# Optimization experiments

Measured on AMD Instinct MI355X. Metric: run time of the kernel, lower is better.

Reference implementation:

```python
import jax, jax.numpy as jnp
import numpy as np

EMBED_DIM = 768
NUM_HEADS = 12


def setup_inputs() -> dict:
    key = jax.random.key(0)
    ks = jax.random.split(key, 9)
    B, N, C = 16, 1024, EMBED_DIM
    std = 1.0 / np.sqrt(C)
    x = jax.random.normal(ks[0], (B, N, C), dtype=jnp.float32)
    def w(k):
        return jax.random.normal(k, (C, C), dtype=jnp.float32) * std
    def b(k):
        return jax.random.normal(k, (C,), dtype=jnp.float32) * 0.01
    return {
        "x": x,
        "Wq": w(ks[1]), "bq": b(ks[2]),
        "Wk": w(ks[3]), "bk": b(ks[4]),
        "Wv": w(ks[5]), "bv": b(ks[6]),
        "Wo": w(ks[7]), "bo": b(ks[8]),
    }


def reference(x, Wq, bq, Wk, bk, Wv, bv, Wo, bo):
    B, N, C = x.shape
    H = NUM_HEADS
    Dh = C // H
    scale = 1.0 / np.sqrt(Dh)

    q = x @ Wq + bq  # (B, N, C)
    k = x @ Wk + bk
    v = x @ Wv + bv

    # Faithful to the original: (B, N, H, Dh) -> reshape(B*H, N, Dh)
    # WITHOUT transposing, exactly as torch_mla_core does (row-major reshape).
    q2 = q.reshape(B * H, N, Dh)
    k2 = k.reshape(B * H, N, Dh)
    v2 = v.reshape(B * H, N, Dh)

    scores = jnp.einsum('gld,gmd->glm', q2, k2) * scale  # (B*H, N, N)
    attn = jax.nn.softmax(scores, axis=-1)
    ctx2 = jnp.einsum('glm,gmd->gld', attn, v2)  # (B*H, N, Dh)

    ctx = ctx2.reshape(B, H, N, Dh).transpose(0, 2, 1, 3).reshape(B, N, C)
    out = ctx @ Wo + bo
    return out
```

## Files before the change

### kernel.cpp

```cpp
#include <hip/hip_runtime.h>
#include <hip/hip_bf16.h>
#include <cstdint>
#include <cstddef>

typedef unsigned short u16;
typedef __attribute__((ext_vector_type(8))) short s8v;
typedef __attribute__((ext_vector_type(4))) float f4v;
typedef __attribute__((ext_vector_type(8))) u16 u16x8;
typedef __attribute__((ext_vector_type(4))) uint32_t u32x4;

#define AS1 __attribute__((address_space(1)))
#define AS3 __attribute__((address_space(3)))

#define BATCH 16
#define SEQ   1024
#define EMBED 768
#define HEADS 12
#define DH    64
#define MTOT  (BATCH*SEQ)

__device__ __forceinline__ u16 f2bf(float f) {
    union { float f; uint32_t u; } v; v.f = f;
    uint32_t r = v.u + 0x7fffu + ((v.u >> 16) & 1u);
    return (u16)(r >> 16);
}

__device__ __forceinline__ void gll16(const u16* g, u16* l) {
    __builtin_amdgcn_global_load_lds((AS1 void*)g, (AS3 void*)l, 16, 0, 0);
}

#define XBLOCKS 12288
#define TBLOCKS 576
__global__ void k_pack(const float* __restrict__ x, u16* __restrict__ xb, int nx,
                       const float* __restrict__ Wq, const float* __restrict__ Wk,
                       const float* __restrict__ Wv, const float* __restrict__ Wo,
                       const float* __restrict__ bq, const float* __restrict__ bk,
                       const float* __restrict__ bv,
                       u16* __restrict__ wqkvT, u16* __restrict__ woT,
                       float* __restrict__ bqkv)
{
    __shared__ __attribute__((aligned(16))) u16 ts[64 * 80];
    const int tid = threadIdx.x;
    if (blockIdx.x < XBLOCKS) {
        int i = (blockIdx.x * 256 + tid) * 4;
        if (i + 3 < nx) {
            float4 f = *(const float4*)(x + i);
            ushort4 o;
            o.x = f2bf(f.x); o.y = f2bf(f.y); o.z = f2bf(f.z); o.w = f2bf(f.w);
            *(ushort4*)(xb + i) = o;
        }
        return;
    }
    int tb = blockIdx.x - XBLOCKS;
    if (tb < TBLOCKS) {
        const float* src; u16* dst; int n0, k0, nn0; float sc;
        if (tb < 432) {
            int nt = tb % 36, kt = tb / 36;
            n0 = nt * 64; k0 = kt * 64; dst = wqkvT;
            if (n0 < 768)       { src = Wq; nn0 = n0;        sc = 0.125f; }
            else if (n0 < 1536) { src = Wk; nn0 = n0 - 768;  sc = 1.0f;   }
            else                { src = Wv; nn0 = n0 - 1536; sc = 1.0f;   }
        } else {
            int tb2 = tb - 432;
            int nt = tb2 % 12, kt = tb2 / 12;
            n0 = nt * 64; k0 = kt * 64; nn0 = n0; sc = 1.0f;
            src = Wo; dst = woT;
        }
        const int r = tid >> 2, cb = (tid & 3) * 16;
#pragma unroll
        for (int i = 0; i < 4; ++i) {
            float4 f = *(const float4*)(src + (size_t)(k0 + r) * 768 + nn0 + cb + i * 4);
            ts[(cb + i * 4 + 0) * 80 + r] = f2bf(f.x * sc);
            ts[(cb + i * 4 + 1) * 80 + r] = f2bf(f.y * sc);
            ts[(cb + i * 4 + 2) * 80 + r] = f2bf(f.z * sc);
            ts[(cb + i * 4 + 3) * 80 + r] = f2bf(f.w * sc);
        }
        __syncthreads();
#pragma unroll
        for (int j = 0; j < 2; ++j) {
            u16x8 tv = *(const u16x8*)(ts + r * 80 + cb + j * 8);
            *(u16x8*)(dst + (size_t)(n0 + r) * 768 + k0 + cb + j * 8) = tv;
        }
        return;
    }
    int t3 = (tb - TBLOCKS) * 256 + tid;
    if (t3 < 2304) {
        bqkv[t3] = (t3 < 768) ? bq[t3] * 0.125f
                 : ((t3 < 1536) ? bk[t3 - 768] : bv[t3 - 1536]);
    }
}

template<int MODE>
__global__ __launch_bounds__(256) void k_gemm(
    const u16* __restrict__ A, const u16* __restrict__ BT,
    const float* __restrict__ bias,
    u16* __restrict__ oq, u16* __restrict__ okk, u16* __restrict__ ov,
    float* __restrict__ of)
{
    __shared__ __attribute__((aligned(16))) u16 As[128 * 64];
    __shared__ __attribute__((aligned(16))) u16 Bs[128 * 64];
    const int tid = threadIdx.x;
    const int m0 = blockIdx.x * 128;
    const int n0 = blockIdx.y * 128;
    const int wv = tid >> 6;
    const int ln = tid & 63;
    const int l15 = ln & 15, quad = ln >> 4;
    const int wm = (wv >> 1) * 64, wn = (wv & 1) * 64;

    const int srow = tid >> 3;
    const int schnk = ((tid & 7) ^ (srow & 7)) * 8;
    const u16* gA = A + (size_t)(m0 + srow) * 768 + schnk;
    const u16* gB = BT + (size_t)(n0 + srow) * 768 + schnk;
    u16* lA = As + wv * 512;
    u16* lB = Bs + wv * 512;

    const int sl0 = ((quad)     ^ (l15 & 7)) * 8;
    const int sl1 = ((4 + quad) ^ (l15 & 7)) * 8;

    f4v acc[4][4] = {};

    for (int kt = 0; kt < 12; ++kt) {
        const int ko = kt * 64;
#pragma unroll
        for (int i = 0; i < 4; ++i) {
            gll16(gA + (size_t)i * 32 * 768 + ko, lA + i * 2048);
            gll16(gB + (size_t)i * 32 * 768 + ko, lB + i * 2048);
        }
        __syncthreads();

        s8v aF[4][2];
#pragma unroll
        for (int i = 0; i < 4; ++i) {
            const u16* base = As + (wm + i * 16 + l15) * 64;
            aF[i][0] = *(const s8v*)(base + sl0);
            aF[i][1] = *(const s8v*)(base + sl1);
        }
#pragma unroll
        for (int j = 0; j < 4; ++j) {
            const u16* base = Bs + (wn + j * 16 + l15) * 64;
            s8v bF0 = *(const s8v*)(base + sl0);
            s8v bF1 = *(const s8v*)(base + sl1);
#pragma unroll
            for (int i = 0; i < 4; ++i) {
                acc[i][j] = __builtin_amdgcn_mfma_f32_16x16x32_bf16(aF[i][0], bF0, acc[i][j], 0, 0, 0);
                acc[i][j] = __builtin_amdgcn_mfma_f32_16x16x32_bf16(aF[i][1], bF1, acc[i][j], 0, 0, 0);
            }
        }
        __syncthreads();
    }

#pragma unroll
    for (int j = 0; j < 4; ++j) {
        int n = n0 + wn + j * 16 + l15;
        float bs = bias[n];
        if (MODE == 0) {
            u16* dst; int nn;
            if (n < 768)       { dst = oq;  nn = n; }
            else if (n < 1536) { dst = okk; nn = n - 768; }
            else               { dst = ov;  nn = n - 1536; }
#pragma unroll
            for (int i = 0; i < 4; ++i) {
                int mrow = m0 + wm + i * 16 + quad * 4;
#pragma unroll
                for (int rg = 0; rg < 4; ++rg)
                    dst[(size_t)(mrow + rg) * 768 + nn] = f2bf(acc[i][j][rg] + bs);
            }
        } else {
#pragma unroll
            for (int i = 0; i < 4; ++i) {
                int mrow = m0 + wm + i * 16 + quad * 4;
#pragma unroll
                for (int rg = 0; rg < 4; ++rg)
                    of[(size_t)(mrow + rg) * 768 + n] = acc[i][j][rg] + bs;
            }
        }
    }
}

__global__ void k_transpose_v(const u16* __restrict__ v, u16* __restrict__ vt) {
    __shared__ __attribute__((aligned(16))) u16 ts[64 * 80];
    int g = blockIdx.x >> 4;
    int l0 = (blockIdx.x & 15) << 6;
    const u16* vg = v + (size_t)g * 65536;
    u16* vtg = vt + (size_t)g * 65536;
    int tid = threadIdx.x;
#pragma unroll
    for (int c = tid; c < 512; c += 256) {
        int l = c >> 3, d0 = (c & 7) * 8;
        *(uint4*)(ts + l * 80 + d0) = *(const uint4*)(vg + (size_t)(l0 + l) * 64 + d0);
    }
    __syncthreads();
#pragma unroll
    for (int c = tid; c < 512; c += 256) {
        int d = c >> 3, lc = (c & 7) * 8;
        u16x8 tv;
#pragma unroll
        for (int i = 0; i < 8; ++i) tv[i] = ts[(lc + i) * 80 + d];
        *(u16x8*)(vtg + (size_t)d * 1024 + l0 + lc) = tv;
    }
}

#define KS2(r_, c_) ( ((r_) << 6) + (((((c_) >> 3) ^ ((r_) & 7)) & 7) << 3) + ((c_) & 7) )

__global__ __launch_bounds__(256) void k_attn(
    const u16* __restrict__ qb, const u16* __restrict__ kb,
    const u16* __restrict__ vt, u16* __restrict__ ctx)
{
    __shared__ __attribute__((aligned(16))) u16 Ks[128 * 64];
    __shared__ __attribute__((aligned(16))) u16 Vts[64 * 136];

    const int g = blockIdx.x >> 3;
    const int q0 = (blockIdx.x & 7) << 7;
    const int tid = threadIdx.x, wv = tid >> 6;
    const int ln = tid & 63, l15 = ln & 15, quad = ln >> 4;
    const u16* qg = qb + (size_t)g * 65536;
    const u16* kg = kb + (size_t)g * 65536;
    const u16* vtg = vt + (size_t)g * 65536;

    const int krr = tid >> 3, kcb = (tid & 7) * 8;
    const int vd = tid >> 4, vc0 = (tid & 15) * 8;
    const u16* kgp = kg + (size_t)krr * 64 + kcb;
    const u16* vgp = vtg + (size_t)vd * 1024 + vc0;

    uint4 kr0 = *(const uint4*)(kgp);
    uint4 kr1 = *(const uint4*)(kgp + 2048);
    uint4 kr2 = *(const uint4*)(kgp + 4096);
    uint4 kr3 = *(const uint4*)(kgp + 6144);
    uint4 vr0 = *(const uint4*)(vgp);
    uint4 vr1 = *(const uint4*)(vgp + 16384);
    uint4 vr2 = *(const uint4*)(vgp + 32768);
    uint4 vr3 = *(const uint4*)(vgp + 49152);

    const u16* qrow = qg + (size_t)(q0 + wv * 32 + l15) * 64 + quad * 8;
    s8v aQ00 = *(const s8v*)qrow;
    s8v aQ01 = *(const s8v*)(qrow + 32);
    s8v aQ10 = *(const s8v*)(qrow + 1024);
    s8v aQ11 = *(const s8v*)(qrow + 1024 + 32);

    f4v o0[4] = {}, o1[4] = {};
    float rsum0 = 0.f, rsum1 = 0.f;

    for (int jt = 0; jt < 8; ++jt) {
        __builtin_amdgcn_s_barrier();
        __builtin_amdgcn_sched_barrier(0);

        *(uint4*)(Ks + KS2(krr,      kcb)) = kr0;
        *(uint4*)(Ks + KS2(krr + 32, kcb)) = kr1;
        *(uint4*)(Ks + KS2(krr + 64, kcb)) = kr2;
        *(uint4*)(Ks + KS2(krr + 96, kcb)) = kr3;
        *(uint4*)(Vts + (vd     ) * 136 + vc0) = vr0;
        *(uint4*)(Vts + (vd + 16) * 136 + vc0) = vr1;
        *(uint4*)(Vts + (vd + 32) * 136 + vc0) = vr2;
        *(uint4*)(Vts + (vd + 48) * 136 + vc0) = vr3;

        if (jt < 7) {
            const size_t koff = (size_t)(jt + 1) * 8192;
            const int voff = (jt + 1) * 128;
            kr0 = *(const uint4*)(kgp + koff);
            kr1 = *(const uint4*)(kgp + koff + 2048);
            kr2 = *(const uint4*)(kgp + koff + 4096);
            kr3 = *(const uint4*)(kgp + koff + 6144);
            vr0 = *(const uint4*)(vgp + voff);
            vr1 = *(const uint4*)(vgp + voff + 16384);
            vr2 = *(const uint4*)(vgp + voff + 32768);
            vr3 = *(const uint4*)(vgp + voff + 49152);
        }

        asm volatile("s_waitcnt lgkmcnt(0)" ::: "memory");
        __builtin_amdgcn_s_barrier();
        __builtin_amdgcn_sched_barrier(0);

        f4v s0[8], s1[8];
        __builtin_amdgcn_s_setprio(1);
#pragma unroll
        for (int ns = 0; ns < 8; ++ns) {
            int rK = ns * 16 + l15;
            s8v b0 = *(const s8v*)(Ks + KS2(rK, quad * 8));
            s8v b1 = *(const s8v*)(Ks + KS2(rK, quad * 8 + 32));
            f4v t0 = {};
            t0 = __builtin_amdgcn_mfma_f32_16x16x32_bf16(b0, aQ00, t0, 0, 0, 0);
            t0 = __builtin_amdgcn_mfma_f32_16x16x32_bf16(b1, aQ01, t0, 0, 0, 0);
            s0[ns] = t0;
            f4v t1 = {};
            t1 = __builtin_amdgcn_mfma_f32_16x16x32_bf16(b0, aQ10, t1, 0, 0, 0);
            t1 = __builtin_amdgcn_mfma_f32_16x16x32_bf16(b1, aQ11, t1, 0, 0, 0);
            s1[ns] = t1;
        }
        __builtin_amdgcn_s_setprio(0);

        s8v aP0[4], aP1[4];
#pragma unroll
        for (int ns = 0; ns < 8; ++ns)
#pragma unroll
            for (int rg = 0; rg < 4; ++rg) {
                float p = __expf(s0[ns][rg]);
                s0[ns][rg] = p;
                rsum0 += p;
            }
#pragma unroll
        for (int ks = 0; ks < 4; ++ks) {
            uint32_t a0, a1, c0, c1;
            asm("v_cvt_pk_bf16_f32 %0, %1, %2" : "=v"(a0) : "v"(s0[2*ks][0]),   "v"(s0[2*ks][1]));
            asm("v_cvt_pk_bf16_f32 %0, %1, %2" : "=v"(a1) : "v"(s0[2*ks][2]),   "v"(s0[2*ks][3]));
            asm("v_cvt_pk_bf16_f32 %0, %1, %2" : "=v"(c0) : "v"(s0[2*ks+1][0]), "v"(s0[2*ks+1][1]));
            asm("v_cvt_pk_bf16_f32 %0, %1, %2" : "=v"(c1) : "v"(s0[2*ks+1][2]), "v"(s0[2*ks+1][3]));
            asm("v_permlane32_swap_b32 %0, %1" : "+v"(a0), "+v"(c0));
            asm("v_permlane16_swap_b32 %0, %1" : "+v"(a0), "+v"(c0));
            asm("v_permlane32_swap_b32 %0, %1" : "+v"(a1), "+v"(c1));
            asm("v_permlane16_swap_b32 %0, %1" : "+v"(a1), "+v"(c1));
            u32x4 pk; pk.x = a0; pk.y = a1; pk.z = c0; pk.w = c1;
            aP0[ks] = __builtin_bit_cast(s8v, pk);
        }
#pragma unroll
        for (int ns = 0; ns < 8; ++ns)
#pragma unroll
            for (int rg = 0; rg < 4; ++rg) {
                float p = __expf(s1[ns][rg]);
                s1[ns][rg] = p;
                rsum1 += p;
            }
#pragma unroll
        for (int ks = 0; ks < 4; ++ks) {
            uint32_t a0, a1, c0, c1;
            asm("v_cvt_pk_bf16_f32 %0, %1, %2" : "=v"(a0) : "v"(s1[2*ks][0]),   "v"(s1[2*ks][1]));
            asm("v_cvt_pk_bf16_f32 %0, %1, %2" : "=v"(a1) : "v"(s1[2*ks][2]),   "v"(s1[2*ks][3]));
            asm("v_cvt_pk_bf16_f32 %0, %1, %2" : "=v"(c0) : "v"(s1[2*ks+1][0]), "v"(s1[2*ks+1][1]));
            asm("v_cvt_pk_bf16_f32 %0, %1, %2" : "=v"(c1) : "v"(s1[2*ks+1][2]), "v"(s1[2*ks+1][3]));
            asm("v_permlane32_swap_b32 %0, %1" : "+v"(a0), "+v"(c0));
            asm("v_permlane16_swap_b32 %0, %1" : "+v"(a0), "+v"(c0));
            asm("v_permlane32_swap_b32 %0, %1" : "+v"(a1), "+v"(c1));
            asm("v_permlane16_swap_b32 %0, %1" : "+v"(a1), "+v"(c1));
            u32x4 pk; pk.x = a0; pk.y = a1; pk.z = c0; pk.w = c1;
            aP1[ks] = __builtin_bit_cast(s8v, pk);
        }

        __builtin_amdgcn_s_setprio(1);
#pragma unroll
        for (int ks = 0; ks < 4; ++ks)
#pragma unroll
            for (int ds = 0; ds < 4; ++ds) {
                s8v bV = *(const s8v*)(Vts + (ds * 16 + l15) * 136 + ks * 32 + quad * 8);
                o0[ds] = __builtin_amdgcn_mfma_f32_16x16x32_bf16(aP0[ks], bV, o0[ds], 0, 0, 0);
                o1[ds] = __builtin_amdgcn_mfma_f32_16x16x32_bf16(aP1[ks], bV, o1[ds], 0, 0, 0);
            }
        __builtin_amdgcn_s_setprio(0);
    }

    rsum0 += __shfl_xor(rsum0, 16, 64);
    rsum0 += __shfl_xor(rsum0, 32, 64);
    rsum1 += __shfl_xor(rsum1, 16, 64);
    rsum1 += __shfl_xor(rsum1, 32, 64);

    const int b = g / 12, h = g % 12;
    u16* cbase = ctx + (size_t)b * 786432 + h * 64;
#pragma unroll
    for (int rg = 0; rg < 4; ++rg) {
        int row0 = q0 + wv * 32 + quad * 4 + rg;
        float inv0 = 1.0f / __shfl(rsum0, 20 * quad + rg, 64);
#pragma unroll
        for (int ds = 0; ds < 4; ++ds)
            cbase[(size_t)row0 * 768 + ds * 16 + l15] = f2bf(o0[ds][rg] * inv0);
        int row1 = row0 + 16;
        float inv1 = 1.0f / __shfl(rsum1, 20 * quad + rg, 64);
#pragma unroll
        for (int ds = 0; ds < 4; ++ds)
            cbase[(size_t)row1 * 768 + ds * 16 + l15] = f2bf(o1[ds][rg] * inv1);
    }
}

extern "C" void kernel_launch(void* const* d_in, const int* in_sizes, int n_in,
                              void* d_out, int out_size, void* d_ws, size_t ws_size,
                              hipStream_t stream) {
    const float* x  = (const float*)d_in[0];
    const float* Wq = (const float*)d_in[1];
    const float* bq = (const float*)d_in[2];
    const float* Wk = (const float*)d_in[3];
    const float* bk = (const float*)d_in[4];
    const float* Wv = (const float*)d_in[5];
    const float* bv = (const float*)d_in[6];
    const float* Wo = (const float*)d_in[7];
    const float* bo = (const float*)d_in[8];
    float* out = (float*)d_out;

    const size_t NTOK = (size_t)MTOT * EMBED;
    char* w = (char*)d_ws;
    u16* xb    = (u16*)w;              w += NTOK * 2;
    u16* qb    = (u16*)w;              w += NTOK * 2;
    u16* kb    = (u16*)w;              w += NTOK * 2;
    u16* vb    = (u16*)w;              w += NTOK * 2;
    u16* vtb   = (u16*)w;              w += NTOK * 2;
    u16* wqkvT = (u16*)w;              w += (size_t)2304 * 768 * 2;
    u16* woT   = (u16*)w;              w += (size_t)768 * 768 * 2;
    float* bqkv = (float*)w;           w += 2304 * 4;
    u16* ctx = xb;

    k_pack<<<XBLOCKS + TBLOCKS + 9, 256, 0, stream>>>(x, xb, (int)NTOK,
        Wq, Wk, Wv, Wo, bq, bk, bv, wqkvT, woT, bqkv);

    dim3 g1(128, 18);
    k_gemm<0><<<g1, 256, 0, stream>>>(xb, wqkvT, bqkv, qb, kb, vb, nullptr);

    k_transpose_v<<<3072, 256, 0, stream>>>(vb, vtb);
    k_attn<<<1536, 256, 0, stream>>>(qb, kb, vtb, ctx);

    dim3 g2(128, 6);
    k_gemm<1><<<g2, 256, 0, stream>>>(ctx, woT, bo, nullptr, nullptr, nullptr, out);
}
```

Measured before the change: 329.3 us.

## Fold log2e into Q scale, use hardware exp2, compute row sums via MFMA

Scales Q by log2(e)/sqrt(Dh) so the softmax exponent can use a raw v_exp_f32 instead of __expf, removing a multiply per element. Row sums are no longer accumulated in scalar VALU adds and reduced with shuffles. Instead an extra MFMA against a row of bf16 ones in LDS accumulates them alongside P·V, with the sums taken from the bf16-rounded probabilities. Block-to-(head, query tile) mapping is also reordered, presumably to improve cache locality or spread work across XCDs.

```diff
diff --git a/kernel.cpp b/kernel.cpp
--- a/kernel.cpp
+++ b/kernel.cpp
@@ -18,11 +18,18 @@
 #define HEADS 12
 #define DH    64
 #define MTOT  (BATCH*SEQ)
+#define QSCALE 0.1803368867f
 
 __device__ __forceinline__ u16 f2bf(float f) {
     union { float f; uint32_t u; } v; v.f = f;
     uint32_t r = v.u + 0x7fffu + ((v.u >> 16) & 1u);
     return (u16)(r >> 16);
+}
+
+__device__ __forceinline__ float exp2_hw(float x) {
+    float r;
+    asm("v_exp_f32 %0, %1" : "=v"(r) : "v"(x));
+    return r;
 }
 
 __device__ __forceinline__ void gll16(const u16* g, u16* l) {
@@ -57,7 +64,7 @@
         if (tb < 432) {
             int nt = tb % 36, kt = tb / 36;
             n0 = nt * 64; k0 = kt * 64; dst = wqkvT;
-            if (n0 < 768)       { src = Wq; nn0 = n0;        sc = 0.125f; }
+            if (n0 < 768)       { src = Wq; nn0 = n0;        sc = QSCALE; }
             else if (n0 < 1536) { src = Wk; nn0 = n0 - 768;  sc = 1.0f;   }
             else                { src = Wv; nn0 = n0 - 1536; sc = 1.0f;   }
         } else {
@@ -85,7 +92,7 @@
     }
     int t3 = (tb - TBLOCKS) * 256 + tid;
     if (t3 < 2304) {
-        bqkv[t3] = (t3 < 768) ? bq[t3] * 0.125f
+        bqkv[t3] = (t3 < 768) ? bq[t3] * QSCALE
                  : ((t3 < 1536) ? bk[t3 - 768] : bv[t3 - 1536]);
     }
 }
@@ -207,10 +214,12 @@
     const u16* __restrict__ vt, u16* __restrict__ ctx)
 {
     __shared__ __attribute__((aligned(16))) u16 Ks[128 * 64];
-    __shared__ __attribute__((aligned(16))) u16 Vts[64 * 136];
-
-    const int g = blockIdx.x >> 3;
-    const int q0 = (blockIdx.x & 7) << 7;
+    __shared__ __attribute__((aligned(16))) u16 Vts[80 * 136];
+
+    const int bid = blockIdx.x;
+    const int xr = bid & 7, bt = bid >> 3;
+    const int g = xr * 24 + (bt >> 3);
+    const int q0 = (bt & 7) << 7;
     const int tid = threadIdx.x, wv = tid >> 6;
     const int ln = tid & 63, l15 = ln & 15, quad = ln >> 4;
     const u16* qg = qb + (size_t)g * 65536;
@@ -231,6 +240,13 @@
     uint4 vr2 = *(const uint4*)(vgp + 32768);
     uint4 vr3 = *(const uint4*)(vgp + 49152);
 
+    if (tid < 16) {
+        uint4 ones;
+        ones.x = 0x3F803F80u; ones.y = 0x3F803F80u;
+        ones.z = 0x3F803F80u; ones.w = 0x3F803F80u;
+        *(uint4*)(Vts + 64 * 136 + tid * 8) = ones;
+    }
+
     const u16* qrow = qg + (size_t)(q0 + wv * 32 + l15) * 64 + quad * 8;
     s8v aQ00 = *(const s8v*)qrow;
     s8v aQ01 = *(const s8v*)(qrow + 32);
@@ -238,7 +254,7 @@
     s8v aQ11 = *(const s8v*)(qrow + 1024 + 32);
 
     f4v o0[4] = {}, o1[4] = {};
-    float rsum0 = 0.f, rsum1 = 0.f;
+    f4v o4_0 = {}, o4_1 = {};
 
     for (int jt = 0; jt < 8; ++jt) {
         __builtin_amdgcn_s_barrier();
@@ -292,11 +308,8 @@
 #pragma unroll
         for (int ns = 0; ns < 8; ++ns)
 #pragma unroll
-            for (int rg = 0; rg < 4; ++rg) {
-                float p = __expf(s0[ns][rg]);
-                s0[ns][rg] = p;
-                rsum0 += p;
-            }
+            for (int rg = 0; rg < 4; ++rg)
+                s0[ns][rg] = exp2_hw(s0[ns][rg]);
 #pragma unroll
         for (int ks = 0; ks < 4; ++ks) {
             uint32_t a0, a1, c0, c1;
@@ -314,11 +327,8 @@
 #pragma unroll
         for (int ns = 0; ns < 8; ++ns)
 #pragma unroll
-            for (int rg = 0; rg < 4; ++rg) {
-                float p = __expf(s1[ns][rg]);
-                s1[ns][rg] = p;
-                rsum1 += p;
-            }
+            for (int rg = 0; rg < 4; ++rg)
+                s1[ns][rg] = exp2_hw(s1[ns][rg]);
 #pragma unroll
         for (int ks = 0; ks < 4; ++ks) {
             uint32_t a0, a1, c0, c1;
@@ -336,32 +346,31 @@
 
         __builtin_amdgcn_s_setprio(1);
 #pragma unroll
-        for (int ks = 0; ks < 4; ++ks)
+        for (int ks = 0; ks < 4; ++ks) {
 #pragma unroll
             for (int ds = 0; ds < 4; ++ds) {
                 s8v bV = *(const s8v*)(Vts + (ds * 16 + l15) * 136 + ks * 32 + quad * 8);
                 o0[ds] = __builtin_amdgcn_mfma_f32_16x16x32_bf16(aP0[ks], bV, o0[ds], 0, 0, 0);
                 o1[ds] = __builtin_amdgcn_mfma_f32_16x16x32_bf16(aP1[ks], bV, o1[ds], 0, 0, 0);
             }
+            s8v bV4 = *(const s8v*)(Vts + (64 + l15) * 136 + ks * 32 + quad * 8);
+            o4_0 = __builtin_amdgcn_mfma_f32_16x16x32_bf16(aP0[ks], bV4, o4_0, 0, 0, 0);
+            o4_1 = __builtin_amdgcn_mfma_f32_16x16x32_bf16(aP1[ks], bV4, o4_1, 0, 0, 0);
+        }
         __builtin_amdgcn_s_setprio(0);
     }
-
-    rsum0 += __shfl_xor(rsum0, 16, 64);
-    rsum0 += __shfl_xor(rsum0, 32, 64);
-    rsum1 += __shfl_xor(rsum1, 16, 64);
-    rsum1 += __shfl_xor(rsum1, 32, 64);
 
     const int b = g / 12, h = g % 12;
     u16* cbase = ctx + (size_t)b * 786432 + h * 64;
 #pragma unroll
     for (int rg = 0; rg < 4; ++rg) {
         int row0 = q0 + wv * 32 + quad * 4 + rg;
-        float inv0 = 1.0f / __shfl(rsum0, 20 * quad + rg, 64);
+        float inv0 = 1.0f / __shfl(o4_0[rg], quad << 4, 64);
 #pragma unroll
         for (int ds = 0; ds < 4; ++ds)
             cbase[(size_t)row0 * 768 + ds * 16 + l15] = f2bf(o0[ds][rg] * inv0);
         int row1 = row0 + 16;
-        float inv1 = 1.0f / __shfl(rsum1, 20 * quad + rg, 64);
+        float inv1 = 1.0f / __shfl(o4_1[rg], quad << 4, 64);
 #pragma unroll
         for (int ds = 0; ds < 4; ++ds)
             cbase[(size_t)row1 * 768 + ds * 16 + l15] = f2bf(o1[ds][rg] * inv1);
```

After: 303.7 us. 1.08x faster.
